# Kernel tuning notes

Measured on AMD Instinct MI355X. Metric: run time of the kernel, lower is better.

## Reference

```python
import jax, jax.numpy as jnp
import numpy as np

D_MODEL = 512
NUM_HEADS = 8
D_K = D_MODEL // NUM_HEADS


def _linear(x, w, b):
    # torch nn.Linear: y = x @ w.T + b, w: [out, in]
    return jnp.einsum('bsd,ed->bse', x, w) + b


def _attn_proj(x, w1, b1, w2, b2):
    return jax.nn.silu(_linear(x, w1, b1)) * _linear(x, w2, b2)


def setup_inputs() -> dict:
    key = jax.random.key(0)
    ks = jax.random.split(key, 20)
    B, S, D = 4, 8192, D_MODEL
    scale = 1.0 / np.sqrt(D)
    inp = {
        'query': jax.random.normal(ks[0], (B, S, D), jnp.float32),
        'key': jax.random.normal(ks[1], (B, S, D), jnp.float32),
        'value': jax.random.normal(ks[2], (B, S, D), jnp.float32),
    }
    names = ['q_w1', 'q_w2', 'k_w1', 'k_w2', 'v_w1', 'v_w2', 'out_w']
    for i, n in enumerate(names):
        inp[n] = jax.random.normal(ks[3 + i], (D, D), jnp.float32) * scale
    bnames = ['q_b1', 'q_b2', 'k_b1', 'k_b2', 'v_b1', 'v_b2', 'out_b']
    for i, n in enumerate(bnames):
        inp[n] = jax.random.normal(ks[10 + i], (D,), jnp.float32) * 0.01
    return inp


def reference(query, key, value,
              q_w1, q_w2, k_w1, k_w2, v_w1, v_w2, out_w,
              q_b1, q_b2, k_b1, k_b2, v_b1, v_b2, out_b):
    B = query.shape[0]
    eps = 1e-6
    # projections -> [B, H, S, d_k]
    def split_heads(x):
        return x.reshape(B, -1, NUM_HEADS, D_K).transpose(0, 2, 1, 3)
    q = split_heads(_attn_proj(query, q_w1, q_b1, q_w2, q_b2))
    k = split_heads(_attn_proj(key, k_w1, k_b1, k_w2, k_b2))
    v = split_heads(_attn_proj(value, v_w1, v_b1, v_w2, v_b2))

    phi_q = jax.nn.elu(q) + 1.0
    phi_k = jax.nn.elu(k) + 1.0
    # key_value: [B, H, d_k, d_k]
    key_value = jnp.einsum('bhsd,bhse->bhde', phi_k, v)
    key_sum = phi_k.sum(axis=-2)                       # [B, H, d_k]
    qk_sum = jnp.einsum('bhsd,bhd->bhs', phi_q, key_sum)
    numerator = jnp.einsum('bhsd,bhde->bhse', phi_q, key_value)
    attn = numerator / (qk_sum[..., None] + eps)       # [B, H, S, d_k]

    x = attn.transpose(0, 2, 1, 3).reshape(B, -1, NUM_HEADS * D_K)
    return _linear(x, out_w, out_b)
```

## Files before the change

### kernel.cpp

```cpp
#include <hip/hip_runtime.h>
#include <stdint.h>


#define DMODEL 512
#define NHEAD 8
#define BATCH 4
#define SEQ 8192
#define BSROWS (BATCH * SEQ)
#define NSPLIT 16
#define CHUNK (SEQ / NSPLIT)

typedef __attribute__((ext_vector_type(8))) short short8;
typedef __attribute__((ext_vector_type(4))) short short4v;
typedef __attribute__((ext_vector_type(4))) float f32x4;
typedef __attribute__((ext_vector_type(4))) unsigned short ushort4v;

__device__ __forceinline__ unsigned short f2bf(float f) {
  union { float f; uint32_t u; } v; v.f = f;
  uint32_t u = v.u;
  u += 0x7fffu + ((u >> 16) & 1u);
  return (unsigned short)(u >> 16);
}
__device__ __forceinline__ float bf2f(unsigned short h) {
  union { float f; uint32_t u; } v; v.u = ((uint32_t)h) << 16; return v.f;
}
__device__ __forceinline__ f32x4 zero4() {
  f32x4 z; z[0] = 0.f; z[1] = 0.f; z[2] = 0.f; z[3] = 0.f; return z;
}
__device__ __forceinline__ void gload_lds16(const unsigned short* g, unsigned short* l) {
  __builtin_amdgcn_global_load_lds((const __attribute__((address_space(1))) void*)g,
                                   (__attribute__((address_space(3))) void*)l, 16, 0, 0);
}

struct WPtrs { const float* w[7]; };

__global__ void convert_weights_kernel(WPtrs wp, unsigned short* __restrict__ wbf) {
  int gid = blockIdx.x * 256 + threadIdx.x;
  int which = gid >> 16;
  int rem = gid & 65535;
  float4 v = ((const float4*)wp.w[which])[rem];
  ushort4v o;
  o[0] = f2bf(v.x); o[1] = f2bf(v.y); o[2] = f2bf(v.z); o[3] = f2bf(v.w);
  *(ushort4v*)(wbf + (size_t)which * 262144 + (size_t)rem * 4) = o;
}

__global__ void convert_x_kernel(const float* __restrict__ q, const float* __restrict__ k,
                                 const float* __restrict__ v, unsigned short* __restrict__ xbf) {
  size_t t = (size_t)blockIdx.x * 256 + threadIdx.x;
  int which = (int)(t >> 21);
  size_t rem = t & 2097151;
  const float* src = which == 0 ? q : (which == 1 ? k : v);
  const float4* s4 = (const float4*)src + rem * 2;
  float4 a = s4[0], b = s4[1];
  short8 o;
  o[0] = (short)f2bf(a.x); o[1] = (short)f2bf(a.y);
  o[2] = (short)f2bf(a.z); o[3] = (short)f2bf(a.w);
  o[4] = (short)f2bf(b.x); o[5] = (short)f2bf(b.y);
  o[6] = (short)f2bf(b.z); o[7] = (short)f2bf(b.w);
  *(short8*)(xbf + ((size_t)which << 24) + rem * 8) = o;
}

struct ProjArgs {
  const float* b1[3];
  const float* b2[3];
  unsigned short* out[3];
};

__global__ __launch_bounds__(1024, 4) void proj_kernel(ProjArgs pa,
                                                       const unsigned short* __restrict__ wbf,
                                                       const unsigned short* __restrict__ xbf) {
  const int which = blockIdx.y;
  const unsigned short* __restrict__ x = xbf + ((size_t)which << 24);
  const unsigned short* __restrict__ w1 = wbf + (size_t)which * 524288;
  const unsigned short* __restrict__ w2 = w1 + 262144;
  const float* __restrict__ b1p = pa.b1[which];
  const float* __restrict__ b2p = pa.b2[which];
  unsigned short* __restrict__ outp = pa.out[which];
  const bool PHI = (which < 2);

  const int wg = (blockIdx.x & 7) * 64 + (blockIdx.x >> 3);
  const int mt = wg >> 2, nt = wg & 3;
  const int m0 = mt * 256, n0 = nt * 128;
  const int tid = threadIdx.x;
  const int wave = tid >> 6, lane = tid & 63;
  const int lrow = lane & 15, quad = lane >> 4;
  const int m_off = (wave >> 2) * 64;
  const int n_off = (wave & 3) * 32;

  __shared__ unsigned short lds[2 * 32768];

  const int srow_l = lane >> 3;
  const int kq_l = (lane & 7) ^ srow_l;
  const int swz = lrow & 7;

  f32x4 acc1[4][2], acc2[4][2];
#pragma unroll
  for (int i = 0; i < 4; i++)
#pragma unroll
    for (int j = 0; j < 2; j++) { acc1[i][j] = zero4(); acc2[i][j] = zero4(); }

  auto stage = [&](unsigned short* dst, int k0) {
#pragma unroll
    for (int i = 0; i < 2; i++) {
      int ig = wave * 2 + i;
      gload_lds16(x + (size_t)(m0 + ig * 8 + srow_l) * 512 + k0 + kq_l * 8,
                  dst + ig * 512);
    }
    size_t roff = (size_t)(n0 + wave * 8 + srow_l) * 512 + k0 + kq_l * 8;
    gload_lds16(w1 + roff, dst + 16384 + wave * 512);
    gload_lds16(w2 + roff, dst + 24576 + wave * 512);
  };

  stage(lds, 0);

  for (int t = 0; t < 8; ++t) {
    unsigned short* cur = lds + (t & 1) * 32768;
    if (t < 7) {
      stage(lds + ((t + 1) & 1) * 32768, (t + 1) * 64);
      asm volatile("s_waitcnt vmcnt(4)" ::: "memory");
    } else {
      asm volatile("s_waitcnt vmcnt(0)" ::: "memory");
    }
    __builtin_amdgcn_s_barrier();

#pragma unroll
    for (int kk = 0; kk < 64; kk += 32) {
      const int e8 = (kk >> 3) + quad;
      short8 af[4], b1f[2], b2f[2];
#pragma unroll
      for (int mi = 0; mi < 4; mi++)
        af[mi] = *(const short8*)(cur + (m_off + mi * 16 + lrow) * 64 + ((e8 ^ swz) << 3));
#pragma unroll
      for (int ni = 0; ni < 2; ni++) {
        int rr = n_off + ni * 16 + lrow;
        b1f[ni] = *(const short8*)(cur + 16384 + rr * 64 + ((e8 ^ swz) << 3));
        b2f[ni] = *(const short8*)(cur + 24576 + rr * 64 + ((e8 ^ swz) << 3));
      }
#pragma unroll
      for (int ni = 0; ni < 2; ni++)
#pragma unroll
        for (int mi = 0; mi < 4; mi++) {
          acc1[mi][ni] = __builtin_amdgcn_mfma_f32_16x16x32_bf16(af[mi], b1f[ni], acc1[mi][ni], 0, 0, 0);
          acc2[mi][ni] = __builtin_amdgcn_mfma_f32_16x16x32_bf16(af[mi], b2f[ni], acc2[mi][ni], 0, 0, 0);
        }
    }
    __builtin_amdgcn_s_barrier();
  }

  if (which == 0) {
#pragma unroll
    for (int ni = 0; ni < 2; ni++) {
      int n = n0 + n_off + ni * 16 + lrow;
      float bb1 = b1p[n], bb2 = b2p[n];
#pragma unroll
      for (int mi = 0; mi < 4; mi++)
#pragma unroll
        for (int r = 0; r < 4; r++) {
          int m = m0 + m_off + mi * 16 + quad * 4 + r;
          float v1 = acc1[mi][ni][r] + bb1;
          float v2 = acc2[mi][ni][r] + bb2;
          float y = v1 * (1.f / (1.f + __expf(-v1))) * v2;
          y = (y > 0.f) ? (y + 1.f) : __expf(y);
          outp[(size_t)m * 512 + n] = f2bf(y);
        }
    }
  } else {
    const int bI = m0 >> 13;
    const int sb = (m0 & 8191) + m_off + quad * 4;
#pragma unroll
    for (int ni = 0; ni < 2; ni++) {
      int n = n0 + n_off + ni * 16 + lrow;
      float bb1 = b1p[n], bb2 = b2p[n];
      int h = n >> 6, d = n & 63;
      unsigned short* dst0 = outp + (((size_t)bI * 8 + h) * 64 + d) * 8192 + sb;
#pragma unroll
      for (int mi = 0; mi < 4; mi++) {
        short4v o;
#pragma unroll
        for (int r = 0; r < 4; r++) {
          float v1 = acc1[mi][ni][r] + bb1;
          float v2 = acc2[mi][ni][r] + bb2;
          float y = v1 * (1.f / (1.f + __expf(-v1))) * v2;
          if (PHI) y = (y > 0.f) ? (y + 1.f) : __expf(y);
          o[r] = (short)f2bf(y);
        }
        *(short4v*)(dst0 + mi * 16) = o;
      }
    }
  }
}

__global__ __launch_bounds__(256) void kv_kernel(const unsigned short* __restrict__ kT,
                                                 const unsigned short* __restrict__ vT,
                                                 float* __restrict__ kvt_part,
                                                 float* __restrict__ ksum_part) {
  const int chunk = blockIdx.x & (NSPLIT - 1);
  const int bh = blockIdx.x >> 4;
  const int tid = threadIdx.x;
  const int wave = tid >> 6, lane = tid & 63;
  const int lrow = lane & 15, quad = lane >> 4;

  __shared__ float ls_acc[4096];
  __shared__ float ls_ksum[64];
  if (tid < 64) ls_ksum[tid] = 0.f;
#pragma unroll
  for (int i = 0; i < 16; i++) ls_acc[tid + 256 * i] = 0.f;

  const unsigned short* vrow = vT + (size_t)bh * 64 * 8192;
  const unsigned short* krow = kT + (size_t)bh * 64 * 8192;
  const int s_w = chunk * CHUNK + wave * 128;

  short8 ones;
#pragma unroll
  for (int j = 0; j < 8; j++) ones[j] = (short)0x3F80;

  f32x4 acc[4][4], aks[4];
#pragma unroll
  for (int i = 0; i < 4; i++) {
    aks[i] = zero4();
#pragma unroll
    for (int j = 0; j < 4; j++) acc[i][j] = zero4();
  }

  for (int it = 0; it < 4; it++) {
    const int s0 = s_w + it * 32 + quad * 8;
    short8 af[4], bfr[4];
#pragma unroll
    for (int mi = 0; mi < 4; mi++)
      af[mi] = *(const short8*)(vrow + (size_t)(mi * 16 + lrow) * 8192 + s0);
#pragma unroll
    for (int ni = 0; ni < 4; ni++)
      bfr[ni] = *(const short8*)(krow + (size_t)(ni * 16 + lrow) * 8192 + s0);
#pragma unroll
    for (int ni = 0; ni < 4; ni++) {
      aks[ni] = __builtin_amdgcn_mfma_f32_16x16x32_bf16(ones, bfr[ni], aks[ni], 0, 0, 0);
#pragma unroll
      for (int mi = 0; mi < 4; mi++)
        acc[mi][ni] = __builtin_amdgcn_mfma_f32_16x16x32_bf16(af[mi], bfr[ni], acc[mi][ni], 0, 0, 0);
    }
  }

  __syncthreads();
#pragma unroll
  for (int mi = 0; mi < 4; mi++)
#pragma unroll
    for (int ni = 0; ni < 4; ni++)
#pragma unroll
      for (int r = 0; r < 4; r++)
        atomicAdd(&ls_acc[(mi * 16 + quad * 4 + r) * 64 + ni * 16 + lrow], acc[mi][ni][r]);
  if (quad == 0) {
#pragma unroll
    for (int ni = 0; ni < 4; ni++) atomicAdd(&ls_ksum[ni * 16 + lrow], aks[ni][0]);
  }
  __syncthreads();

  float* op = kvt_part + ((size_t)chunk * 32 + bh) * 4096;
#pragma unroll
  for (int i = 0; i < 16; i++) op[tid + 256 * i] = ls_acc[tid + 256 * i];
  if (tid < 64) ksum_part[((size_t)chunk * 32 + bh) * 64 + tid] = ls_ksum[tid];
}

__global__ void kv_reduce_kernel(const float* __restrict__ kvt_part,
                                 const float* __restrict__ ksum_part,
                                 unsigned short* __restrict__ kvT,
                                 unsigned short* __restrict__ ksum_bf) {
  const int bh = blockIdx.x >> 2, seg = blockIdx.x & 3;
  const int idx = seg * 1024 + threadIdx.x * 4;
  float4 s = make_float4(0.f, 0.f, 0.f, 0.f);
#pragma unroll
  for (int c = 0; c < NSPLIT; c++) {
    float4 v = *(const float4*)&kvt_part[((size_t)c * 32 + bh) * 4096 + idx];
    s.x += v.x; s.y += v.y; s.z += v.z; s.w += v.w;
  }
  ushort4v o;
  o[0] = f2bf(s.x); o[1] = f2bf(s.y); o[2] = f2bf(s.z); o[3] = f2bf(s.w);
  *(ushort4v*)(kvT + (size_t)bh * 4096 + idx) = o;
  if (seg == 0 && threadIdx.x < 64) {
    float t = 0.f;
#pragma unroll
    for (int c = 0; c < NSPLIT; c++) t += ksum_part[((size_t)c * 32 + bh) * 64 + threadIdx.x];
    ksum_bf[bh * 64 + threadIdx.x] = f2bf(t);
  }
}

__global__ __launch_bounds__(256) void attn_kernel(const unsigned short* __restrict__ phiQ,
                                                   const unsigned short* __restrict__ kvT,
                                                   const unsigned short* __restrict__ ksum_bf,
                                                   unsigned short* __restrict__ xattn) {
  const int bh = blockIdx.x & 31;
  const int st = blockIdx.x >> 5;
  const int b = bh >> 3, h = bh & 7;
  const int tid = threadIdx.x;
  const int wave = tid >> 6, lane = tid & 63;
  const int lrow = lane & 15, quad = lane >> 4;
  const size_t rowbase = (size_t)b * SEQ + st * 128 + wave * 32;

  f32x4 acc[2][4], aqs[2];
#pragma unroll
  for (int i = 0; i < 2; i++) {
    aqs[i] = zero4();
#pragma unroll
    for (int j = 0; j < 4; j++) acc[i][j] = zero4();
  }

#pragma unroll
  for (int kk = 0; kk < 64; kk += 32) {
    short8 ks = *(const short8*)(ksum_bf + bh * 64 + kk + quad * 8);
    short8 af[2];
#pragma unroll
    for (int mi = 0; mi < 2; mi++)
      af[mi] = *(const short8*)(phiQ + (rowbase + mi * 16 + lrow) * 512 + h * 64 + kk + quad * 8);
#pragma unroll
    for (int mi = 0; mi < 2; mi++)
      aqs[mi] = __builtin_amdgcn_mfma_f32_16x16x32_bf16(af[mi], ks, aqs[mi], 0, 0, 0);
#pragma unroll
    for (int ni = 0; ni < 4; ni++) {
      short8 bfr = *(const short8*)(kvT + (size_t)bh * 4096 + (ni * 16 + lrow) * 64 + kk + quad * 8);
#pragma unroll
      for (int mi = 0; mi < 2; mi++)
        acc[mi][ni] = __builtin_amdgcn_mfma_f32_16x16x32_bf16(af[mi], bfr, acc[mi][ni], 0, 0, 0);
    }
  }
#pragma unroll
  for (int mi = 0; mi < 2; mi++) {
#pragma unroll
    for (int r = 0; r < 4; r++) {
      float inv = 1.f / (aqs[mi][r] + 1e-6f);
      size_t m = rowbase + mi * 16 + quad * 4 + r;
#pragma unroll
      for (int ni = 0; ni < 4; ni++)
        xattn[m * 512 + h * 64 + ni * 16 + lrow] = f2bf(acc[mi][ni][r] * inv);
    }
  }
}

__global__ __launch_bounds__(1024, 4) void out_gemm_kernel(const unsigned short* __restrict__ xattn,
                                                           const unsigned short* __restrict__ wo,
                                                           const float* __restrict__ ob,
                                                           float* __restrict__ out) {
  const int wg = (blockIdx.x & 7) * 64 + (blockIdx.x >> 3);
  const int mt = wg >> 2, nt = wg & 3;
  const int m0 = mt * 256, n0 = nt * 128;
  const int tid = threadIdx.x;
  const int wave = tid >> 6, lane = tid & 63;
  const int lrow = lane & 15, quad = lane >> 4;
  const int m_off = (wave >> 2) * 64;
  const int n_off = (wave & 3) * 32;

  __shared__ unsigned short lds[2 * 24576];

  const int srow_l = lane >> 3;
  const int kq_l = (lane & 7) ^ srow_l;
  const int swz = lrow & 7;

  f32x4 acc[4][2];
#pragma unroll
  for (int i = 0; i < 4; i++)
#pragma unroll
    for (int j = 0; j < 2; j++) acc[i][j] = zero4();

  auto stage = [&](unsigned short* dst, int k0) {
#pragma unroll
    for (int i = 0; i < 2; i++) {
      int ig = wave * 2 + i;
      gload_lds16(xattn + (size_t)(m0 + ig * 8 + srow_l) * 512 + k0 + kq_l * 8,
                  dst + ig * 512);
    }
    gload_lds16(wo + (size_t)(n0 + wave * 8 + srow_l) * 512 + k0 + kq_l * 8,
                dst + 16384 + wave * 512);
  };

  stage(lds, 0);

  for (int t = 0; t < 8; ++t) {
    unsigned short* cur = lds + (t & 1) * 24576;
    if (t < 7) {
      stage(lds + ((t + 1) & 1) * 24576, (t + 1) * 64);
      asm volatile("s_waitcnt vmcnt(3)" ::: "memory");
    } else {
      asm volatile("s_waitcnt vmcnt(0)" ::: "memory");
    }
    __builtin_amdgcn_s_barrier();

#pragma unroll
    for (int kk = 0; kk < 64; kk += 32) {
      const int e8 = (kk >> 3) + quad;
      short8 af[4], bfr[2];
#pragma unroll
      for (int mi = 0; mi < 4; mi++)
        af[mi] = *(const short8*)(cur + (m_off + mi * 16 + lrow) * 64 + ((e8 ^ swz) << 3));
#pragma unroll
      for (int ni = 0; ni < 2; ni++)
        bfr[ni] = *(const short8*)(cur + 16384 + (n_off + ni * 16 + lrow) * 64 + ((e8 ^ swz) << 3));
#pragma unroll
      for (int ni = 0; ni < 2; ni++)
#pragma unroll
        for (int mi = 0; mi < 4; mi++)
          acc[mi][ni] = __builtin_amdgcn_mfma_f32_16x16x32_bf16(af[mi], bfr[ni], acc[mi][ni], 0, 0, 0);
    }
    __builtin_amdgcn_s_barrier();
  }

#pragma unroll
  for (int ni = 0; ni < 2; ni++) {
    int n = n0 + n_off + ni * 16 + lrow;
    float bb = ob[n];
#pragma unroll
    for (int mi = 0; mi < 4; mi++)
#pragma unroll
      for (int r = 0; r < 4; r++) {
        int m = m0 + m_off + mi * 16 + quad * 4 + r;
        out[(size_t)m * 512 + n] = acc[mi][ni][r] + bb;
      }
  }
}

extern "C" void kernel_launch(void* const* d_in, const int* in_sizes, int n_in,
                              void* d_out, int out_size, void* d_ws, size_t ws_size,
                              hipStream_t stream) {
  char* ws = (char*)d_ws;
  size_t off = 0;
  auto alloc = [&](size_t bytes) -> void* {
    void* p = ws + off;
    off += (bytes + 255) & ~(size_t)255;
    return p;
  };
  unsigned short* wbf = (unsigned short*)alloc((size_t)7 * 262144 * 2);
  unsigned short* phiQ = (unsigned short*)alloc((size_t)BSROWS * 512 * 2);
  unsigned short* kT = (unsigned short*)alloc((size_t)BSROWS * 512 * 2);
  unsigned short* vT = (unsigned short*)alloc((size_t)BSROWS * 512 * 2);
  unsigned short* xbf = (unsigned short*)alloc((size_t)3 * BSROWS * 512 * 2);
  if (off > ws_size) return;

  char* xr = (char*)xbf;
  unsigned short* xattn = (unsigned short*)xr;
  float* kvt_part = (float*)(xr + 67108864);
  float* ksum_part = (float*)(xr + 75497472);
  unsigned short* kvT = (unsigned short*)(xr + 75628544);
  unsigned short* ksum_bf = (unsigned short*)(xr + 75890688);

  WPtrs wp;
  for (int i = 0; i < 7; i++) wp.w[i] = (const float*)d_in[3 + i];
  convert_weights_kernel<<<1792, 256, 0, stream>>>(wp, wbf);
  convert_x_kernel<<<24576, 256, 0, stream>>>((const float*)d_in[0], (const float*)d_in[1],
                                              (const float*)d_in[2], xbf);

  ProjArgs pa;
  pa.b1[0] = (const float*)d_in[10]; pa.b2[0] = (const float*)d_in[11];
  pa.b1[1] = (const float*)d_in[12]; pa.b2[1] = (const float*)d_in[13];
  pa.b1[2] = (const float*)d_in[14]; pa.b2[2] = (const float*)d_in[15];
  pa.out[0] = phiQ; pa.out[1] = kT; pa.out[2] = vT;
  proj_kernel<<<dim3(512, 3), 1024, 0, stream>>>(pa, wbf, xbf);

  kv_kernel<<<512, 256, 0, stream>>>(kT, vT, kvt_part, ksum_part);
  kv_reduce_kernel<<<128, 256, 0, stream>>>(kvt_part, ksum_part, kvT, ksum_bf);
  attn_kernel<<<2048, 256, 0, stream>>>(phiQ, kvT, ksum_bf, xattn);
  out_gemm_kernel<<<512, 1024, 0, stream>>>(xattn, wbf + (size_t)6 * 262144,
                                            (const float*)d_in[16], (float*)d_out);
}
```

Before: 477.1 us.

## Fuse fp32-to-bf16 input conversion into projection GEMM staging

Removes the separate convert_x kernel and has the projection kernel read fp32 activations directly, convert them to bf16 in registers, and write them swizzled into LDS. The A-tile loads are issued before the MFMA loop and written to the next buffer afterwards, so the global load latency overlaps compute. This avoids writing and re-reading a 96MB bf16 copy of the inputs and one launch. In exchange the fp32 A loads double the global read bytes per tile inside the GEMM, and the pipeline now waits for all loads with vmcnt(0) every iteration instead of keeping prefetches in flight.

```diff
diff --git a/kernel.cpp b/kernel.cpp
--- a/kernel.cpp
+++ b/kernel.cpp
@@ -44,33 +44,17 @@
   *(ushort4v*)(wbf + (size_t)which * 262144 + (size_t)rem * 4) = o;
 }
 
-__global__ void convert_x_kernel(const float* __restrict__ q, const float* __restrict__ k,
-                                 const float* __restrict__ v, unsigned short* __restrict__ xbf) {
-  size_t t = (size_t)blockIdx.x * 256 + threadIdx.x;
-  int which = (int)(t >> 21);
-  size_t rem = t & 2097151;
-  const float* src = which == 0 ? q : (which == 1 ? k : v);
-  const float4* s4 = (const float4*)src + rem * 2;
-  float4 a = s4[0], b = s4[1];
-  short8 o;
-  o[0] = (short)f2bf(a.x); o[1] = (short)f2bf(a.y);
-  o[2] = (short)f2bf(a.z); o[3] = (short)f2bf(a.w);
-  o[4] = (short)f2bf(b.x); o[5] = (short)f2bf(b.y);
-  o[6] = (short)f2bf(b.z); o[7] = (short)f2bf(b.w);
-  *(short8*)(xbf + ((size_t)which << 24) + rem * 8) = o;
-}
-
 struct ProjArgs {
+  const float* xf[3];
   const float* b1[3];
   const float* b2[3];
   unsigned short* out[3];
 };
 
 __global__ __launch_bounds__(1024, 4) void proj_kernel(ProjArgs pa,
-                                                       const unsigned short* __restrict__ wbf,
-                                                       const unsigned short* __restrict__ xbf) {
+                                                       const unsigned short* __restrict__ wbf) {
   const int which = blockIdx.y;
-  const unsigned short* __restrict__ x = xbf + ((size_t)which << 24);
+  const float* __restrict__ xf = pa.xf[which];
   const unsigned short* __restrict__ w1 = wbf + (size_t)which * 524288;
   const unsigned short* __restrict__ w2 = w1 + 262144;
   const float* __restrict__ b1p = pa.b1[which];
@@ -93,35 +77,53 @@
   const int kq_l = (lane & 7) ^ srow_l;
   const int swz = lrow & 7;
 
+  const int arow_l = wave * 4 + (lane >> 4);
+  const int ac = lane & 15;
+  const int ao8 = ac >> 1, ahalf = ac & 1;
+
   f32x4 acc1[4][2], acc2[4][2];
 #pragma unroll
   for (int i = 0; i < 4; i++)
 #pragma unroll
     for (int j = 0; j < 2; j++) { acc1[i][j] = zero4(); acc2[i][j] = zero4(); }
 
-  auto stage = [&](unsigned short* dst, int k0) {
-#pragma unroll
-    for (int i = 0; i < 2; i++) {
-      int ig = wave * 2 + i;
-      gload_lds16(x + (size_t)(m0 + ig * 8 + srow_l) * 512 + k0 + kq_l * 8,
-                  dst + ig * 512);
-    }
+  float4 a4[4];
+  auto stageA_load = [&](int k0) {
+#pragma unroll
+    for (int j = 0; j < 4; j++) {
+      int row = j * 64 + arow_l;
+      a4[j] = *(const float4*)(xf + (size_t)(m0 + row) * 512 + k0 + ac * 4);
+    }
+  };
+  auto stageA_write = [&](unsigned short* dstA) {
+#pragma unroll
+    for (int j = 0; j < 4; j++) {
+      int row = j * 64 + arow_l;
+      short4v o;
+      o[0] = (short)f2bf(a4[j].x); o[1] = (short)f2bf(a4[j].y);
+      o[2] = (short)f2bf(a4[j].z); o[3] = (short)f2bf(a4[j].w);
+      *(short4v*)(dstA + row * 64 + ((ao8 ^ (row & 7)) << 3) + ahalf * 4) = o;
+    }
+  };
+  auto stageW = [&](unsigned short* dst, int k0) {
     size_t roff = (size_t)(n0 + wave * 8 + srow_l) * 512 + k0 + kq_l * 8;
     gload_lds16(w1 + roff, dst + 16384 + wave * 512);
     gload_lds16(w2 + roff, dst + 24576 + wave * 512);
   };
 
-  stage(lds, 0);
+  stageA_load(0);
+  stageW(lds, 0);
+  stageA_write(lds);
+  asm volatile("s_waitcnt vmcnt(0) lgkmcnt(0)" ::: "memory");
+  __builtin_amdgcn_s_barrier();
 
   for (int t = 0; t < 8; ++t) {
     unsigned short* cur = lds + (t & 1) * 32768;
+    unsigned short* nxt = lds + ((t + 1) & 1) * 32768;
     if (t < 7) {
-      stage(lds + ((t + 1) & 1) * 32768, (t + 1) * 64);
-      asm volatile("s_waitcnt vmcnt(4)" ::: "memory");
-    } else {
-      asm volatile("s_waitcnt vmcnt(0)" ::: "memory");
-    }
-    __builtin_amdgcn_s_barrier();
+      stageA_load((t + 1) * 64);
+      stageW(nxt, (t + 1) * 64);
+    }
 
 #pragma unroll
     for (int kk = 0; kk < 64; kk += 32) {
@@ -144,6 +146,9 @@
           acc2[mi][ni] = __builtin_amdgcn_mfma_f32_16x16x32_bf16(af[mi], b2f[ni], acc2[mi][ni], 0, 0, 0);
         }
     }
+
+    if (t < 7) stageA_write(nxt);
+    asm volatile("s_waitcnt vmcnt(0) lgkmcnt(0)" ::: "memory");
     __builtin_amdgcn_s_barrier();
   }
 
@@ -429,10 +434,9 @@
   unsigned short* phiQ = (unsigned short*)alloc((size_t)BSROWS * 512 * 2);
   unsigned short* kT = (unsigned short*)alloc((size_t)BSROWS * 512 * 2);
   unsigned short* vT = (unsigned short*)alloc((size_t)BSROWS * 512 * 2);
-  unsigned short* xbf = (unsigned short*)alloc((size_t)3 * BSROWS * 512 * 2);
+  char* xr = (char*)alloc((size_t)3 * BSROWS * 512 * 2);
   if (off > ws_size) return;
 
-  char* xr = (char*)xbf;
   unsigned short* xattn = (unsigned short*)xr;
   float* kvt_part = (float*)(xr + 67108864);
   float* ksum_part = (float*)(xr + 75497472);
@@ -442,15 +446,15 @@
   WPtrs wp;
   for (int i = 0; i < 7; i++) wp.w[i] = (const float*)d_in[3 + i];
   convert_weights_kernel<<<1792, 256, 0, stream>>>(wp, wbf);
-  convert_x_kernel<<<24576, 256, 0, stream>>>((const float*)d_in[0], (const float*)d_in[1],
-                                              (const float*)d_in[2], xbf);
 
   ProjArgs pa;
+  pa.xf[0] = (const float*)d_in[0]; pa.xf[1] = (const float*)d_in[1];
+  pa.xf[2] = (const float*)d_in[2];
   pa.b1[0] = (const float*)d_in[10]; pa.b2[0] = (const float*)d_in[11];
   pa.b1[1] = (const float*)d_in[12]; pa.b2[1] = (const float*)d_in[13];
   pa.b1[2] = (const float*)d_in[14]; pa.b2[2] = (const float*)d_in[15];
   pa.out[0] = phiQ; pa.out[1] = kT; pa.out[2] = vT;
-  proj_kernel<<<dim3(512, 3), 1024, 0, stream>>>(pa, wbf, xbf);
+  proj_kernel<<<dim3(512, 3), 1024, 0, stream>>>(pa, wbf);
 
   kv_kernel<<<512, 256, 0, stream>>>(kT, vT, kvt_part, ksum_part);
   kv_reduce_kernel<<<128, 256, 0, stream>>>(kvt_part, ksum_part, kvT, ksum_bf);
```

After: 460.6 us. 3.5% less time.
